# Performance work log

Hardware: AMD Instinct MI355X
Metric: run time of the kernel (lower is better)

## Reference

```python
import jax, jax.numpy as jnp
import numpy as np

LMAX = 6
BLOCK_SIZES = [(2 * l + 1) ** 2 for l in range(LMAX + 1)]  # [1,9,25,49,81,121,169], sum=455
IRREPS_DIM = sum(BLOCK_SIZES)


def setup_inputs() -> dict:
    key = jax.random.key(0)
    k1, k2, k3 = jax.random.split(key, 3)
    B, F_IN, F_OUT, N_GRID = 256, 128, 128, 512
    x = jax.random.normal(k1, (B, F_IN, IRREPS_DIM), dtype=jnp.float32)
    w = jax.random.normal(k2, (F_IN, F_OUT, N_GRID), dtype=jnp.float32)
    D = jax.random.normal(k3, (N_GRID, IRREPS_DIM), dtype=jnp.float32)
    return {"x": x, "w": w, "D": D}


def _so3_linear(x, psi):
    # x: [B, f_in, 455], psi: [f_in, f_out, 455]
    # Per-degree grouped linear: for each l, input block is (mul=2l+1, dim=2l+1),
    # weight block is (mul_in=2l+1, mul_out=2l+1); e3nn normalization 1/sqrt(f_in*mul_in).
    B, f_in, _ = x.shape
    f_out = psi.shape[1]
    outs = []
    off = 0
    for l in range(LMAX + 1):
        d = 2 * l + 1
        sz = d * d
        xb = x[:, :, off:off + sz].reshape(B, f_in, d, d)          # [B,f,u,i]
        wb = psi[:, :, off:off + sz].reshape(f_in, f_out, d, d)    # [f,g,u,v]
        yb = jnp.einsum('bfui,fguv->bgvi', xb, wb) / np.sqrt(f_in * d).astype(np.float32)
        outs.append(yb.reshape(B, f_out, sz))
        off += sz
    return jnp.concatenate(outs, axis=-1)  # [B, f_out, 455]


def reference(x, w, D):
    n_grid = D.shape[0]
    # Kernel synthesis from Wigner-D buffer: psi[f,g,i] = sum_n D[n,i] * w[f,g,n] / sqrt(n_grid)
    psi = jnp.einsum('ni,xyn->xyi', D, w) / np.float32(np.sqrt(n_grid))
    return _so3_linear(x, psi)
```

## Files before the change

kernel.cpp:

```cpp
#include <hip/hip_runtime.h>
#include <math.h>


typedef float f32x4 __attribute__((ext_vector_type(4)));
typedef short short8 __attribute__((ext_vector_type(8)));
typedef short short4v __attribute__((ext_vector_type(4)));
typedef __bf16 bf8 __attribute__((ext_vector_type(8)));

static __device__ inline bf8 as_bf8(short8 s) {
    union { short8 s; bf8 b; } u; u.s = s; return u.b;
}
static __device__ inline short f2bf(float f) {
    union { float f; unsigned u; } v; v.f = f;
    unsigned r = v.u + 0x7FFFu + ((v.u >> 16) & 1u);
    return (short)(r >> 16);
}
static __device__ __forceinline__ void glds16(const short* g, short* l) {
    __builtin_amdgcn_global_load_lds(
        (const __attribute__((address_space(1))) unsigned*)g,
        (__attribute__((address_space(3))) unsigned*)l, 16, 0, 0);
}

static const int OFFS_H[8] = {0, 1, 10, 35, 84, 165, 286, 455};
static const size_t PSIOFF_H[7] = {0, 16384, 163840, 573440, 1376256, 2703360, 4685824};
static constexpr unsigned PSIOFF_C[7] = {0, 16384, 163840, 573440, 1376256, 2703360, 4685824};
static constexpr unsigned XPOFF_C[7] = {0, 32768, 327680, 1146880, 2752512, 5406720, 9371648};
__constant__ int OFFS_D[8] = {0, 1, 10, 35, 84, 165, 286, 455};
__constant__ unsigned PSIOFF_D[7] = {0, 16384, 163840, 573440, 1376256, 2703360, 4685824};
__constant__ unsigned XPOFF_D[7] = {0, 32768, 327680, 1146880, 2752512, 5406720, 9371648};

__global__ void transpose_D(const float* __restrict__ D, short* __restrict__ DT) {
    int idx = blockIdx.x * 256 + threadIdx.x;
    if (idx >= 455 * 512) return;
    int n = idx & 511, c = idx >> 9;
    DT[(size_t)c * 512 + n] = f2bf(D[(size_t)n * 455 + c]);
}

static __device__ __forceinline__ void psi_body(int rawid, const float* __restrict__ w,
                                                const short* __restrict__ DT,
                                                short* __restrict__ PSIall,
                                                short (*As)[72], short (*Bs)[72],
                                                int* colInfo) {
    int id = (rawid & 7) * 128 + (rawid >> 3);
    const int nt = id & 3, mt = id >> 2;
    const int tid = threadIdx.x, wave = tid >> 6, lane = tid & 63;
    const int wm = (wave & 1) * 32, wn = (wave >> 1) * 64;

    if (tid < 128) {
        int cp = nt * 128 + tid;
        int info = -1;
        if (cp < 455) {
            int l = 6;
            while (OFFS_D[l] > cp) --l;
            int t = cp - OFFS_D[l];
            int d = 2 * l + 1;
            int v = t / d, u = t - v * d;
            info = (OFFS_D[l] + u * d + v) | (u << 9) | (v << 13) | (l << 17);
        }
        colInfo[tid] = info;
    }
    __syncthreads();

    int brow[4];
#pragma unroll
    for (int c = 0; c < 4; ++c) {
        int inf = colInfo[(tid + c * 256) >> 3];
        brow[c] = (inf < 0) ? 0 : (inf & 511);
    }

    const float* Ag = w + (size_t)(mt * 64) * 512;
    f32x4 acc[2][4] = {};

    for (int k0 = 0; k0 < 512; k0 += 64) {
        __syncthreads();
#pragma unroll
        for (int c = 0; c < 4; ++c) {
            int e = (tid + c * 256) * 4;
            int r = e >> 6, cc = e & 63;
            float4 v = *reinterpret_cast<const float4*>(Ag + (size_t)r * 512 + k0 + cc);
            short4v s;
            s.x = f2bf(v.x); s.y = f2bf(v.y); s.z = f2bf(v.z); s.w = f2bf(v.w);
            *reinterpret_cast<short4v*>(&As[r][cc]) = s;
        }
#pragma unroll
        for (int c = 0; c < 4; ++c) {
            int ch = tid + c * 256;
            int r = ch >> 3, cc = (ch & 7) * 8;
            short8 v = *reinterpret_cast<const short8*>(DT + (size_t)brow[c] * 512 + k0 + cc);
            *reinterpret_cast<short8*>(&Bs[r][cc]) = v;
        }
        __syncthreads();
#pragma unroll
        for (int kf = 0; kf < 2; ++kf) {
            const int kc = kf * 32 + (lane >> 4) * 8;
            short8 af[2], bfr[4];
#pragma unroll
            for (int mi = 0; mi < 2; ++mi)
                af[mi] = *reinterpret_cast<const short8*>(&As[wm + mi * 16 + (lane & 15)][kc]);
#pragma unroll
            for (int ni = 0; ni < 4; ++ni)
                bfr[ni] = *reinterpret_cast<const short8*>(&Bs[wn + ni * 16 + (lane & 15)][kc]);
#pragma unroll
            for (int mi = 0; mi < 2; ++mi)
#pragma unroll
                for (int ni = 0; ni < 4; ++ni)
                    acc[mi][ni] = __builtin_amdgcn_mfma_f32_16x16x32_bf16(
                        as_bf8(af[mi]), as_bf8(bfr[ni]), acc[mi][ni], 0, 0, 0);
        }
    }

    const float s1 = 0.044194173824159216f;
    const int f = mt >> 1;
#pragma unroll
    for (int mi = 0; mi < 2; ++mi)
#pragma unroll
        for (int ni = 0; ni < 4; ++ni) {
            int inf = colInfo[wn + ni * 16 + (lane & 15)];
            if (inf >= 0) {
                int u = (inf >> 9) & 15, v = (inf >> 13) & 15, l = (inf >> 17) & 7;
                int d = 2 * l + 1;
                size_t base = PSIOFF_D[l];
#pragma unroll
                for (int r = 0; r < 4; ++r) {
                    int m = mt * 64 + wm + mi * 16 + (lane >> 4) * 4 + r;
                    int g = m & 127;
                    PSIall[base + (size_t)(g * d + v) * (128 * d) + f * d + u] =
                        f2bf(acc[mi][ni][r] * s1);
                }
            }
        }
}

template <int l>
static __device__ __forceinline__ void pack_body_t(int local, const float* __restrict__ x,
                                                   short* __restrict__ XPl,
                                                   short (*Ls)[170]) {
    constexpr int d = 2 * l + 1;
    constexpr int sz = d * d;
    constexpr int K = 128 * d;
    constexpr int off = l * (2 * l - 1) * (2 * l + 1) / 3;
    const int fc = local & 3, b = local >> 2;
    const int tid = threadIdx.x;
    const float* xb = x + ((size_t)b * 128 + fc * 32) * 455 + off;
    constexpr int total = 32 * sz;
    for (int e = tid; e < total; e += 256) {
        int ff = e / sz, t = e - ff * sz;
        Ls[ff][t] = f2bf(xb[(size_t)ff * 455 + t]);
    }
    __syncthreads();
    constexpr int row = 32 * d;
    for (int e = tid; e < total; e += 256) {
        int i = e / row;
        int rem = e - i * row;
        int ff = rem / d, u = rem - ff * d;
        XPl[((size_t)b * d + i) * K + (fc * 32 + ff) * d + u] = Ls[ff][u * d + i];
    }
}

__global__ __launch_bounds__(256) void prep_all(const float* __restrict__ w,
                                                const short* __restrict__ DT,
                                                const float* __restrict__ x,
                                                short* __restrict__ PSIall,
                                                short* __restrict__ XPall) {
    __shared__ __align__(16) char smem[28160];
    const int bid = blockIdx.x;
    if (bid < 1024) {
        short (*As)[72] = (short(*)[72])smem;
        short (*Bs)[72] = (short(*)[72])(smem + 9216);
        int* colInfo = (int*)(smem + 27648);
        psi_body(bid, w, DT, PSIall, As, Bs, colInfo);
    } else {
        const int id = bid - 1024;
        const int lj = id >> 10;
        const int local = id & 1023;
        short (*Ls)[170] = (short(*)[170])smem;
        switch (lj) {
            case 0: pack_body_t<6>(local, x, XPall + XPOFF_C[6], Ls); break;
            case 1: pack_body_t<5>(local, x, XPall + XPOFF_C[5], Ls); break;
            case 2: pack_body_t<4>(local, x, XPall + XPOFF_C[4], Ls); break;
            case 3: pack_body_t<3>(local, x, XPall + XPOFF_C[3], Ls); break;
            case 4: pack_body_t<2>(local, x, XPall + XPOFF_C[2], Ls); break;
            case 5: pack_body_t<1>(local, x, XPall + XPOFF_C[1], Ls); break;
            default: pack_body_t<0>(local, x, XPall + XPOFF_C[0], Ls); break;
        }
    }
}

__global__ __launch_bounds__(256) void psi_gemm_all(const float* __restrict__ w,
                                                    const short* __restrict__ DT,
                                                    short* __restrict__ PSIall) {
    __shared__ short As[64][72];
    __shared__ short Bs[128][72];
    __shared__ int colInfo[128];
    psi_body(blockIdx.y * gridDim.x + blockIdx.x, w, DT, PSIall, As, Bs, colInfo);
}

template <int d>
__global__ __launch_bounds__(256) void pack_x(const float* __restrict__ x,
                                              short* __restrict__ XP, int off) {
    constexpr int sz = d * d;
    constexpr int K = 128 * d;
    const int fc = blockIdx.x, b = blockIdx.y;
    __shared__ short Ls[64][sz + 1];
    const int tid = threadIdx.x;
    const float* xb = x + ((size_t)b * 128 + fc * 64) * 455 + off;
    for (int e = tid; e < 64 * sz; e += 256) {
        int ff = e / sz, t = e - ff * sz;
        Ls[ff][t] = f2bf(xb[(size_t)ff * 455 + t]);
    }
    __syncthreads();
    for (int e = tid; e < 64 * sz; e += 256) {
        int i = e / (64 * d);
        int rem = e - i * (64 * d);
        int ff = rem / d, u = rem - ff * d;
        XP[((size_t)b * d + i) * K + (fc * 64 + ff) * d + u] = Ls[ff][u * d + i];
    }
}

template <int d>
__global__ __launch_bounds__(256) void psi_gemm(const float* __restrict__ w,
                                                const short* __restrict__ DT,
                                                short* __restrict__ PSI, int off) {
    constexpr int sz = d * d;
    constexpr int KP = 128 * d;
    const int mt = blockIdx.x;
    const int nt = blockIdx.y;
    const int tid = threadIdx.x, wave = tid >> 6, lane = tid & 63;
    const int wm = (wave & 1) * 32, wn = (wave >> 1) * 64;

    __shared__ short As[64][72];
    __shared__ short Bs[128][72];

    const float* Ag = w + (size_t)(mt * 64) * 512;
    f32x4 acc[2][4] = {};

    for (int k0 = 0; k0 < 512; k0 += 64) {
        __syncthreads();
#pragma unroll
        for (int c = 0; c < 4; ++c) {
            int e = (tid + c * 256) * 4;
            int r = e >> 6, cc = e & 63;
            float4 v = *reinterpret_cast<const float4*>(Ag + (size_t)r * 512 + k0 + cc);
            short4v s;
            s.x = f2bf(v.x); s.y = f2bf(v.y); s.z = f2bf(v.z); s.w = f2bf(v.w);
            *reinterpret_cast<short4v*>(&As[r][cc]) = s;
        }
#pragma unroll
        for (int c = 0; c < 4; ++c) {
            int ch = tid + c * 256;
            int r = ch >> 3, cc = (ch & 7) * 8;
            int gc = nt * 128 + r;
            int row = off + (gc < sz ? gc : 0);
            short8 v = *reinterpret_cast<const short8*>(DT + (size_t)row * 512 + k0 + cc);
            *reinterpret_cast<short8*>(&Bs[r][cc]) = v;
        }
        __syncthreads();
#pragma unroll
        for (int kf = 0; kf < 2; ++kf) {
            const int kc = kf * 32 + (lane >> 4) * 8;
            short8 af[2], bfr[4];
#pragma unroll
            for (int mi = 0; mi < 2; ++mi)
                af[mi] = *reinterpret_cast<const short8*>(&As[wm + mi * 16 + (lane & 15)][kc]);
#pragma unroll
            for (int ni = 0; ni < 4; ++ni)
                bfr[ni] = *reinterpret_cast<const short8*>(&Bs[wn + ni * 16 + (lane & 15)][kc]);
#pragma unroll
            for (int mi = 0; mi < 2; ++mi)
#pragma unroll
                for (int ni = 0; ni < 4; ++ni)
                    acc[mi][ni] = __builtin_amdgcn_mfma_f32_16x16x32_bf16(
                        as_bf8(af[mi]), as_bf8(bfr[ni]), acc[mi][ni], 0, 0, 0);
        }
    }

    const float s1 = 0.044194173824159216f;
#pragma unroll
    for (int mi = 0; mi < 2; ++mi)
#pragma unroll
        for (int ni = 0; ni < 4; ++ni) {
            int cix = nt * 128 + wn + ni * 16 + (lane & 15);
            if (cix < sz) {
                int u = cix / d, v = cix - u * d;
#pragma unroll
                for (int r = 0; r < 4; ++r) {
                    int m = mt * 64 + wm + mi * 16 + (lane >> 4) * 4 + r;
                    int f = m >> 7, g = m & 127;
                    PSI[(size_t)(g * d + v) * KP + f * d + u] = f2bf(acc[mi][ni][r] * s1);
                }
            }
        }
}

template <int l>
static __device__ __forceinline__ void so3_body(int pp,
                                                const short* __restrict__ XPall,
                                                const short* __restrict__ PSIall,
                                                float* __restrict__ out,
                                                short (*As)[64 * 64],
                                                short (*Bs)[128 * 64]) {
    constexpr int d = 2 * l + 1;
    constexpr int K = 128 * d;
    constexpr int NT = K / 64;
    constexpr int S = 4 * d * d;
    constexpr int q = S >> 3;
    constexpr int off = l * (2 * l - 1) * (2 * l + 1) / 3;
    constexpr int mtiles = 2 * d;

    const int xcd = pp & 7, pos = pp >> 3;
    const int local = (xcd < 4 ? xcd * (q + 1) : 4 * (q + 1) + (xcd - 4) * q) + pos;
    const int mt = local % mtiles, nt = local / mtiles;

    const int tid = threadIdx.x, wave = tid >> 6, lane = tid & 63;
    const int wm = (wave & 1) * 32, wn = (wave >> 1) * 64;

    const short* Ag = PSIall + PSIOFF_C[l] + (size_t)(mt * 64) * K;
    const short* Bg = XPall + XPOFF_C[l] + (size_t)(nt * 128) * K;

    const int lrow = lane >> 3;
    const int scol = (((lane & 7) ^ lrow) << 3);

    f32x4 acc[2][4] = {};

#define STAGE(buf, k0s)                                                          \
    {                                                                            \
        _Pragma("unroll")                                                        \
        for (int c = 0; c < 2; ++c)                                              \
            glds16(Ag + (size_t)(wave * 16 + 8 * c + lrow) * K + (k0s) + scol,   \
                   &As[buf][(wave * 16 + 8 * c) * 64]);                          \
        _Pragma("unroll")                                                        \
        for (int c = 0; c < 4; ++c)                                              \
            glds16(Bg + (size_t)(wave * 32 + 8 * c + lrow) * K + (k0s) + scol,   \
                   &Bs[buf][(wave * 32 + 8 * c) * 64]);                          \
    }

#define COMPUTE(buf)                                                             \
    {                                                                            \
        _Pragma("unroll")                                                        \
        for (int kf = 0; kf < 2; ++kf) {                                         \
            const int so = (((kf * 4 + (lane >> 4)) ^ (lane & 7)) << 3);         \
            short8 af[2], bfr[4];                                                \
            _Pragma("unroll")                                                    \
            for (int mi = 0; mi < 2; ++mi)                                       \
                af[mi] = *reinterpret_cast<const short8*>(                       \
                    &As[buf][(wm + mi * 16 + (lane & 15)) * 64 + so]);           \
            _Pragma("unroll")                                                    \
            for (int ni = 0; ni < 4; ++ni)                                       \
                bfr[ni] = *reinterpret_cast<const short8*>(                      \
                    &Bs[buf][(wn + ni * 16 + (lane & 15)) * 64 + so]);           \
            _Pragma("unroll")                                                    \
            for (int mi = 0; mi < 2; ++mi)                                       \
                _Pragma("unroll")                                                \
                for (int ni = 0; ni < 4; ++ni)                                   \
                    acc[mi][ni] = __builtin_amdgcn_mfma_f32_16x16x32_bf16(       \
                        as_bf8(af[mi]), as_bf8(bfr[ni]), acc[mi][ni], 0, 0, 0);  \
        }                                                                        \
    }

    STAGE(0, 0);
#pragma unroll 1
    for (int t = 0; t < NT; t += 2) {
        STAGE(1, (t + 1) * 64);
        asm volatile("s_waitcnt vmcnt(6)" ::: "memory");
        __builtin_amdgcn_s_barrier();
        COMPUTE(0);
        __builtin_amdgcn_s_barrier();
        if (t + 2 < NT) {
            STAGE(0, (t + 2) * 64);
            asm volatile("s_waitcnt vmcnt(6)" ::: "memory");
        } else {
            asm volatile("s_waitcnt vmcnt(0)" ::: "memory");
        }
        __builtin_amdgcn_s_barrier();
        COMPUTE(1);
        __builtin_amdgcn_s_barrier();
    }
#undef STAGE
#undef COMPUTE

    constexpr float s2v = 1.0f / (11.313708498984761f);
    (void)s2v;
    const float s2 = rsqrtf(128.0f * (float)d);
#pragma unroll
    for (int mi = 0; mi < 2; ++mi)
#pragma unroll
        for (int ni = 0; ni < 4; ++ni) {
            int n = nt * 128 + wn + ni * 16 + (lane & 15);
            int b = n / d, i = n - b * d;
#pragma unroll
            for (int r = 0; r < 4; ++r) {
                int m = mt * 64 + wm + mi * 16 + (lane >> 4) * 4 + r;
                int g = m / d, v = m - g * d;
                out[((size_t)b * 128 + g) * 455 + off + v * d + i] = acc[mi][ni][r] * s2;
            }
        }
}

__global__ __launch_bounds__(256) void so3_gemm_all(const short* __restrict__ XPall,
                                                    const short* __restrict__ PSIall,
                                                    float* __restrict__ out) {
    __shared__ short As[2][64 * 64];
    __shared__ short Bs[2][128 * 64];
    const int p = blockIdx.x;
    if (p < 676)       so3_body<6>(p,        XPall, PSIall, out, As, Bs);
    else if (p < 1160) so3_body<5>(p - 676,  XPall, PSIall, out, As, Bs);
    else if (p < 1484) so3_body<4>(p - 1160, XPall, PSIall, out, As, Bs);
    else if (p < 1680) so3_body<3>(p - 1484, XPall, PSIall, out, As, Bs);
    else if (p < 1780) so3_body<2>(p - 1680, XPall, PSIall, out, As, Bs);
    else if (p < 1816) so3_body<1>(p - 1780, XPall, PSIall, out, As, Bs);
    else               so3_body<0>(p - 1816, XPall, PSIall, out, As, Bs);
}

template <int d>
__global__ __launch_bounds__(256) void so3_gemm_fb(const short* __restrict__ XP,
                                                   const short* __restrict__ PSI,
                                                   float* __restrict__ out, int off) {
    constexpr int K = 128 * d;
    constexpr int GX = 2 * d;
    constexpr int NWG = 4 * d * d;
    int id = blockIdx.y * gridDim.x + blockIdx.x;
    {
        constexpr int q = NWG >> 3, rr = NWG & 7;
        int xcd = id & 7, pos = id >> 3;
        id = (xcd < rr ? xcd * (q + 1) : rr * (q + 1) + (xcd - rr) * q) + pos;
    }
    const int mt = id % GX, nt = id / GX;
    const int tid = threadIdx.x, wave = tid >> 6, lane = tid & 63;
    const int wm = (wave & 1) * 32, wn = (wave >> 1) * 64;

    __shared__ short As[64][72];
    __shared__ short Bs[128][72];

    const short* Ag = PSI + (size_t)(mt * 64) * K;
    const short* Bg = XP + (size_t)(nt * 128) * K;
    f32x4 acc[2][4] = {};

    for (int k0 = 0; k0 < K; k0 += 64) {
        __syncthreads();
#pragma unroll
        for (int c = 0; c < 2; ++c) {
            int ch = tid + c * 256;
            int r = ch >> 3, cc = (ch & 7) * 8;
            *reinterpret_cast<short8*>(&As[r][cc]) =
                *reinterpret_cast<const short8*>(Ag + (size_t)r * K + k0 + cc);
        }
#pragma unroll
        for (int c = 0; c < 4; ++c) {
            int ch = tid + c * 256;
            int r = ch >> 3, cc = (ch & 7) * 8;
            *reinterpret_cast<short8*>(&Bs[r][cc]) =
                *reinterpret_cast<const short8*>(Bg + (size_t)r * K + k0 + cc);
        }
        __syncthreads();
#pragma unroll
        for (int kf = 0; kf < 2; ++kf) {
            const int kc = kf * 32 + (lane >> 4) * 8;
            short8 af[2], bfr[4];
#pragma unroll
            for (int mi = 0; mi < 2; ++mi)
                af[mi] = *reinterpret_cast<const short8*>(&As[wm + mi * 16 + (lane & 15)][kc]);
#pragma unroll
            for (int ni = 0; ni < 4; ++ni)
                bfr[ni] = *reinterpret_cast<const short8*>(&Bs[wn + ni * 16 + (lane & 15)][kc]);
#pragma unroll
            for (int mi = 0; mi < 2; ++mi)
#pragma unroll
                for (int ni = 0; ni < 4; ++ni)
                    acc[mi][ni] = __builtin_amdgcn_mfma_f32_16x16x32_bf16(
                        as_bf8(af[mi]), as_bf8(bfr[ni]), acc[mi][ni], 0, 0, 0);
        }
    }

    const float s2 = rsqrtf(128.0f * (float)d);
#pragma unroll
    for (int mi = 0; mi < 2; ++mi)
#pragma unroll
        for (int ni = 0; ni < 4; ++ni) {
            int n = nt * 128 + wn + ni * 16 + (lane & 15);
            int b = n / d, i = n - b * d;
#pragma unroll
            for (int r = 0; r < 4; ++r) {
                int m = mt * 64 + wm + mi * 16 + (lane >> 4) * 4 + r;
                int g = m / d, v = m - g * d;
                out[((size_t)b * 128 + g) * 455 + off + v * d + i] = acc[mi][ni][r] * s2;
            }
        }
}

template <int l>
static void run_l_fb(const float* x, const float* w, const short* DT, short* PSIbase,
                     short* XP, float* out, bool fused, hipStream_t stream) {
    constexpr int d = 2 * l + 1;
    const int off = OFFS_H[l];
    if (!fused) {
        constexpr int sz = d * d;
        constexpr int ntiles = (sz + 127) / 128;
        psi_gemm<d><<<dim3(256, ntiles), 256, 0, stream>>>(w, DT, PSIbase, off);
    }
    pack_x<d><<<dim3(2, 256), 256, 0, stream>>>(x, XP, off);
    const short* P = fused ? (PSIbase + PSIOFF_H[l]) : PSIbase;
    so3_gemm_fb<d><<<dim3(2 * d, 2 * d), 256, 0, stream>>>(XP, P, out, off);
}

extern "C" void kernel_launch(void* const* d_in, const int* in_sizes, int n_in,
                              void* d_out, int out_size, void* d_ws, size_t ws_size,
                              hipStream_t stream) {
    const float* x = (const float*)d_in[0];
    const float* w = (const float*)d_in[1];
    const float* D = (const float*)d_in[2];
    float* out = (float*)d_out;

    char* ws = (char*)d_ws;
    const size_t dtBytes      = (size_t)455 * 512 * 2;
    const size_t psiAllBytes  = (size_t)7454720 * 2;
    const size_t psiSlotBytes = (size_t)1664 * 1664 * 2;
    const size_t xpL6Bytes    = (size_t)3328 * 1664 * 2;
    const size_t xpAllBytes   = (size_t)14909440 * 2;

    short* DT = (short*)ws;
    transpose_D<<<(455 * 512 + 255) / 256, 256, 0, stream>>>(D, DT);

    if (ws_size >= dtBytes + psiAllBytes + xpAllBytes) {
        short* PSIall = (short*)(ws + dtBytes);
        short* XPall  = (short*)(ws + dtBytes + psiAllBytes);
        prep_all<<<dim3(8192), 256, 0, stream>>>(w, DT, x, PSIall, XPall);
        so3_gemm_all<<<dim3(1820), 256, 0, stream>>>(XPall, PSIall, out);
        return;
    }

    const bool fused = ws_size >= dtBytes + psiAllBytes + xpL6Bytes;
    short* PSIbase = (short*)(ws + dtBytes);
    short* XP = (short*)(ws + dtBytes + (fused ? psiAllBytes : psiSlotBytes));
    if (fused)
        psi_gemm_all<<<dim3(4, 256), 256, 0, stream>>>(w, DT, PSIbase);

    run_l_fb<0>(x, w, DT, PSIbase, XP, out, fused, stream);
    run_l_fb<1>(x, w, DT, PSIbase, XP, out, fused, stream);
    run_l_fb<2>(x, w, DT, PSIbase, XP, out, fused, stream);
    run_l_fb<3>(x, w, DT, PSIbase, XP, out, fused, stream);
    run_l_fb<4>(x, w, DT, PSIbase, XP, out, fused, stream);
    run_l_fb<5>(x, w, DT, PSIbase, XP, out, fused, stream);
    run_l_fb<6>(x, w, DT, PSIbase, XP, out, fused, stream);
}
```

Baseline: 121.9 us.

## Deepen global-to-LDS pipeline from double to triple buffering

Switches the per-block GEMM main loop from two LDS buffers to three, so two K-tiles are in flight while one is computed. The wait counts are relaxed so each phase waits only for the oldest stage. The intent is to hide more global-load latency behind the MFMA work. In exchange, LDS per block rises from 48KB to 72KB, which may cut how many blocks fit per CU.

```diff
diff --git a/kernel.cpp b/kernel.cpp
--- a/kernel.cpp
+++ b/kernel.cpp
@@ -357,29 +357,33 @@
         }                                                                        \
     }
 
+#define PHASE(b, tc, sb)                                                         \
+    {                                                                            \
+        if ((tc) + 2 < NT) {                                                     \
+            STAGE(sb, ((tc) + 2) * 64);                                          \
+            asm volatile("s_waitcnt vmcnt(12)" ::: "memory");                    \
+        } else if ((tc) + 1 < NT) {                                              \
+            asm volatile("s_waitcnt vmcnt(6)" ::: "memory");                     \
+        } else {                                                                 \
+            asm volatile("s_waitcnt vmcnt(0)" ::: "memory");                     \
+        }                                                                        \
+        __builtin_amdgcn_s_barrier();                                            \
+        COMPUTE(b);                                                              \
+        __builtin_amdgcn_s_barrier();                                            \
+    }
+
     STAGE(0, 0);
+    STAGE(1, 64);
 #pragma unroll 1
-    for (int t = 0; t < NT; t += 2) {
-        STAGE(1, (t + 1) * 64);
-        asm volatile("s_waitcnt vmcnt(6)" ::: "memory");
-        __builtin_amdgcn_s_barrier();
-        COMPUTE(0);
-        __builtin_amdgcn_s_barrier();
-        if (t + 2 < NT) {
-            STAGE(0, (t + 2) * 64);
-            asm volatile("s_waitcnt vmcnt(6)" ::: "memory");
-        } else {
-            asm volatile("s_waitcnt vmcnt(0)" ::: "memory");
-        }
-        __builtin_amdgcn_s_barrier();
-        COMPUTE(1);
-        __builtin_amdgcn_s_barrier();
+    for (int t = 0; t < NT; t += 3) {
+        PHASE(0, t, 2);
+        if (t + 1 < NT) PHASE(1, t + 1, 0);
+        if (t + 2 < NT) PHASE(2, t + 2, 1);
     }
 #undef STAGE
 #undef COMPUTE
-
-    constexpr float s2v = 1.0f / (11.313708498984761f);
-    (void)s2v;
+#undef PHASE
+
     const float s2 = rsqrtf(128.0f * (float)d);
 #pragma unroll
     for (int mi = 0; mi < 2; ++mi)
@@ -399,8 +403,8 @@
 __global__ __launch_bounds__(256) void so3_gemm_all(const short* __restrict__ XPall,
                                                     const short* __restrict__ PSIall,
                                                     float* __restrict__ out) {
-    __shared__ short As[2][64 * 64];
-    __shared__ short Bs[2][128 * 64];
+    __shared__ short As[3][64 * 64];
+    __shared__ short Bs[3][128 * 64];
     const int p = blockIdx.x;
     if (p < 676)       so3_body<6>(p,        XPall, PSIall, out, As, Bs);
     else if (p < 1160) so3_body<5>(p - 676,  XPall, PSIall, out, As, Bs);
```

After: 130.3 us. 6.9% more time.
